# Kernel optimization log

Measured on AMD Instinct MI355X. Metric: run time of the kernel, lower is better.

The kernel has to match this reference:

```python
import jax, jax.numpy as jnp
import numpy as np

NQ = 8
NL = 6
DIM = 2 ** NQ
C64 = jnp.complex64
I2 = jnp.eye(2, dtype=C64)
PX = jnp.array([[0., 1.], [1., 0.]], dtype=C64)
PY = jnp.array([[0., -1j], [1j, 0.]], dtype=C64)
PZ = jnp.array([[1., 0.], [0., -1.]], dtype=C64)
# sign of Pauli-Z eigenvalue for each computational basis state, wires 0..3 (wire 0 = MSB)
_idx = np.arange(DIM)
_SIGNS = jnp.asarray(np.stack([1.0 - 2.0 * ((_idx >> (NQ - 1 - w)) & 1) for w in range(4)]).astype(np.float32))  # (4, 256)

def _rot(t, P):
    # exp(-i t/2 P) = cos(t/2) I - i sin(t/2) P
    th = t.astype(jnp.float32) / 2
    return jnp.cos(th) * I2 - 1j * jnp.sin(th) * P

def _apply1(st, U, w):
    # apply 2x2 unitary U on wire w; st: (B, 2,2,...,2)
    s = jnp.moveaxis(st, w + 1, -1)
    return jnp.moveaxis(s @ U.T, -1, w + 1)

def _cnot(st, c, t):
    # flip target axis where control bit == 1
    s = jnp.moveaxis(st, (c + 1, t + 1), (1, 2))
    s = jnp.concatenate([s[:, :1], s[:, 1:, ::-1]], axis=1)
    return jnp.moveaxis(s, (1, 2), (c + 1, t + 1))

def _quantum(x, weights):
    B = x.shape[0]
    # AmplitudeEmbedding with normalize=True
    psi = (x / jnp.linalg.norm(x, axis=1, keepdims=True)).astype(C64)
    st = psi.reshape((B,) + (2,) * NQ)
    for l in range(NL):
        lw = weights[l]
        for q in range(NQ):
            st = _apply1(st, _rot(lw[3 * q], PX), q)
            st = _apply1(st, _rot(lw[3 * q + 1], PY), q)
            st = _apply1(st, _rot(lw[3 * q + 2], PZ), q)
        for i in range(NQ - 1):
            st = _cnot(st, i, i + 1)
        st = _cnot(st, NQ - 1, 0)
        for i in range(0, NQ, 2):
            if i + 2 < NQ:
                st = _cnot(st, i, i + 2)
    probs = jnp.abs(st.reshape(B, DIM)) ** 2
    return probs @ _SIGNS.T  # (B, 4) Z expectations on wires 0..3

def _bn(h, g, b):
    # BatchNorm1d, training mode (batch statistics, biased variance)
    m = h.mean(0)
    v = h.var(0)
    return g * (h - m) * jax.lax.rsqrt(v + 1e-5) + b

def _forward(x, q_weights, aW, ab, fW1, fb1, fW2, fb2, cW1, cb1, g1, be1, cW2, cb2, g2, be2, cW3, cb3, cW4, cb4):
    q = _quantum(x, q_weights)                     # (B, 4)
    qf = q @ aW.T + ab                             # quantum_adapter
    cf = jnp.tanh(jax.nn.relu(x @ fW1.T + fb1) @ fW2.T + fb2)  # feature_processor
    h = qf + cf
    h = jax.nn.relu(_bn(h @ cW1.T + cb1, g1, be1))
    h = jax.nn.relu(_bn(h @ cW2.T + cb2, g2, be2))
    h = jax.nn.relu(h @ cW3.T + cb3)
    return jax.nn.sigmoid(h @ cW4.T + cb4)         # (B, 1)

def setup_inputs():
    key = jax.random.key(0)
    ks = jax.random.split(key, 21)
    f32 = jnp.float32
    r = lambda k, shp, s: jax.random.normal(k, shp, dtype=f32) * s
    B = 8192
    return {
        'x': r(ks[0], (B, 256), 1.0),
        'q_weights': r(ks[1], (NL, NQ * 3), 1.0),
        'aW': r(ks[2], (4, 4), 0.5), 'ab': r(ks[3], (4,), 0.1),
        'fW1': r(ks[4], (64, 256), 0.0625), 'fb1': r(ks[5], (64,), 0.05),
        'fW2': r(ks[6], (4, 64), 0.125), 'fb2': r(ks[7], (4,), 0.05),
        'cW1': r(ks[8], (32, 4), 0.5), 'cb1': r(ks[9], (32,), 0.05),
        'g1': 1.0 + r(ks[10], (32,), 0.05), 'be1': r(ks[11], (32,), 0.05),
        'cW2': r(ks[12], (16, 32), 0.18), 'cb2': r(ks[13], (16,), 0.05),
        'g2': 1.0 + r(ks[14], (16,), 0.05), 'be2': r(ks[15], (16,), 0.05),
        'cW3': r(ks[16], (8, 16), 0.25), 'cb3': r(ks[17], (8,), 0.05),
        'cW4': r(ks[18], (1, 8), 0.35), 'cb4': r(ks[19], (1,), 0.05),
    }

def reference(x, q_weights, aW, ab, fW1, fb1, fW2, fb2, cW1, cb1, g1, be1, cW2, cb2, g2, be2, cW3, cb3, cW4, cb4):
    return _forward(x, q_weights, aW, ab, fW1, fb1, fW2, fb2, cW1, cb1, g1, be1, cW2, cb2, g2, be2, cW3, cb3, cW4, cb4)
```

## Files before the change

kernel.cpp:

```cpp
#include <hip/hip_runtime.h>
#include <math.h>

#define INV_B (1.0f / 8192.0f)

typedef float  v2f  __attribute__((ext_vector_type(2)));
typedef _Float16 half8 __attribute__((ext_vector_type(8)));
typedef float  f32x4 __attribute__((ext_vector_type(4)));

struct QTables {
    int xm[6][8];
    int rm[6][8];
    int meas[4];
};
constexpr QTables make_tables() {
    QTables T{};
    int Mrow[8] = {}, Ncol[8] = {};
    for (int b = 0; b < 8; ++b) { Mrow[b] = 1 << b; Ncol[b] = 1 << b; }
    constexpr int bc[11] = {7,6,5,4,3,2,1,0,7,5,3};
    constexpr int bt[11] = {6,5,4,3,2,1,0,7,5,3,1};
    for (int l = 0; l < 6; ++l) {
        for (int w = 0; w < 8; ++w) { T.xm[l][w] = Ncol[7 - w]; T.rm[l][w] = Mrow[7 - w]; }
        for (int k = 0; k < 11; ++k) { Mrow[bt[k]] ^= Mrow[bc[k]]; Ncol[bc[k]] ^= Ncol[bt[k]]; }
    }
    for (int w = 0; w < 4; ++w) T.meas[w] = Mrow[7 - w];
    return T;
}
constexpr QTables TB = make_tables();

template<int ML>
static __device__ __forceinline__ float lanex(float v) {
    if constexpr (ML == 0) { return v; }
    else if constexpr (ML == 1) { return __int_as_float(__builtin_amdgcn_update_dpp(0, __float_as_int(v), 0xB1, 0xF, 0xF, true)); }
    else if constexpr (ML == 2) { return __int_as_float(__builtin_amdgcn_update_dpp(0, __float_as_int(v), 0x4E, 0xF, 0xF, true)); }
    else if constexpr (ML == 3) { return __int_as_float(__builtin_amdgcn_update_dpp(0, __float_as_int(v), 0x1B, 0xF, 0xF, true)); }
    else if constexpr (ML < 32) { return __int_as_float(__builtin_amdgcn_ds_swizzle(__float_as_int(v), 0x1F | (ML << 10))); }
    else { return __shfl_xor(v, ML, 64); }
}

static __device__ __forceinline__ float tanh_fast(float v) {
    const float c = fminf(fmaxf(v, -10.f), 10.f);
    const float e = __expf(2.f * c);
    return (e - 1.f) / (e + 1.f);
}

template<int XM, int RM>
static __device__ __forceinline__ void gate(v2f (&z)[4], const int lane,
                                            const float u00r, const float u00i,
                                            const float u01r, const float u01i) {
    constexpr int ML = XM >> 2, MR = XM & 3;
    constexpr int RL = RM >> 2, RR = RM & 3;
    const int pl = __popc(lane & RL) & 1;
    const float csi0 = pl ? -u00i : u00i;
    const float cpr0 = pl ? -u01r : u01r;
    const float csi1 = -csi0, cpr1 = -cpr0;
    v2f p[4];
    #pragma unroll
    for (int r = 0; r < 4; ++r) {
        p[r].x = lanex<ML>(z[r ^ MR].x);
        p[r].y = lanex<ML>(z[r ^ MR].y);
    }
    #pragma unroll
    for (int r = 0; r < 4; ++r) {
        const int pb = __builtin_popcount(r & RR) & 1;
        const float csi = pb ? csi1 : csi0;
        const float cpr = pb ? cpr1 : cpr0;
        const v2f zs = { -z[r].y, z[r].x };
        const v2f ps = { -p[r].y, p[r].x };
        z[r] = ((u00r * z[r] + csi * zs) + cpr * p[r]) + u01i * ps;
    }
}

#define XS 264
__global__ __launch_bounds__(256) void k_pre(
        const float* __restrict__ x, const float* __restrict__ qw,
        const float* __restrict__ fW1, const float* __restrict__ fb1,
        const float* __restrict__ fW2, const float* __restrict__ fb2,
        _Float16* __restrict__ Wt, float* __restrict__ cfws,
        float* __restrict__ accz) {
    const int t = threadIdx.x, b = blockIdx.x;

    if (b >= 128) {
        __shared__ float4 Us[48];
        if (t < 48) {
            const int l = t >> 3, q = t & 7;
            const float* a = qw + l * 24 + q * 3;
            const float h1 = 0.5f * a[0], h2 = 0.5f * a[1], h3 = 0.5f * a[2];
            const float c1 = cosf(h1), s1 = sinf(h1);
            const float c2 = cosf(h2), s2 = sinf(h2);
            const float c3 = cosf(h3), s3 = sinf(h3);
            const float m00r =  c1 * c2, m00i =  s1 * s2;
            const float m01r = -c1 * s2, m01i = -s1 * c2;
            float4 u;
            u.x = m00r * c3 + m00i * s3;  u.y = m00i * c3 - m00r * s3;
            u.z = m01r * c3 + m01i * s3;  u.w = m01i * c3 - m01r * s3;
            Us[t] = u;
        }
        __syncthreads();
        const int lane = t & 63, wv = t >> 6;
        const int k = (b - 128) * 4 + wv;
        v2f z[4];
        #pragma unroll
        for (int r = 0; r < 4; ++r) {
            z[r].x = (4 * lane + r == k) ? 1.f : 0.f;
            z[r].y = 0.f;
        }
#define GATE(L, W) { const float4 u = Us[(L) * 8 + (W)]; \
                     gate<TB.xm[L][W], TB.rm[L][W]>(z, lane, u.x, u.y, u.z, u.w); }
#define LAYER(L) GATE(L,0) GATE(L,1) GATE(L,2) GATE(L,3) GATE(L,4) GATE(L,5) GATE(L,6) GATE(L,7)
        LAYER(0) LAYER(1) LAYER(2) LAYER(3) LAYER(4) LAYER(5)
#undef LAYER
#undef GATE
        #pragma unroll
        for (int r = 0; r < 4; ++r) {
            const int i = 4 * lane + r;
            Wt[(long)i * 256 + k]         = (_Float16)z[r].x;
            Wt[(long)(256 + i) * 256 + k] = (_Float16)z[r].y;
        }
        return;
    }

    if (t < 16) accz[b * 16 + t] = 0.f;

    __shared__ _Float16 xl[64 * XS];
    __shared__ _Float16 wl[64 * XS];
    const long r0 = (long)b * 64;
    #pragma unroll
    for (int i = 0; i < 16; ++i) {
        const int idx = i * 256 + t;
        const int row = idx >> 6, c4 = idx & 63;
        const float4 xv = ((const float4*)(x + (r0 + row) * 256))[c4];
        _Float16* d = &xl[row * XS + c4 * 4];
        d[0] = (_Float16)xv.x; d[1] = (_Float16)xv.y;
        d[2] = (_Float16)xv.z; d[3] = (_Float16)xv.w;
        const float4 wv2 = ((const float4*)(fW1 + (long)row * 256))[c4];
        _Float16* e = &wl[row * XS + c4 * 4];
        e[0] = (_Float16)wv2.x; e[1] = (_Float16)wv2.y;
        e[2] = (_Float16)wv2.z; e[3] = (_Float16)wv2.w;
    }
    __syncthreads();

    const int lane = t & 63, w4 = t >> 6;
    const int g = lane >> 4, col = lane & 15;
    const int rloc = w4 * 16 + col;

    half8 bf[8];
    #pragma unroll
    for (int kb = 0; kb < 8; ++kb)
        bf[kb] = *(const half8*)&xl[rloc * XS + kb * 32 + g * 8];

    float accc[4] = {0.f, 0.f, 0.f, 0.f};
    #pragma unroll
    for (int jc = 0; jc < 4; ++jc) {
        f32x4 cv = {0.f, 0.f, 0.f, 0.f};
        #pragma unroll
        for (int kb = 0; kb < 8; ++kb) {
            const half8 af = *(const half8*)&wl[(jc * 16 + col) * XS + kb * 32 + g * 8];
            cv = __builtin_amdgcn_mfma_f32_16x16x32_f16(af, bf[kb], cv, 0, 0, 0);
        }
        #pragma unroll
        for (int r = 0; r < 4; ++r) {
            const int j = jc * 16 + g * 4 + r;
            const float z = fmaxf(cv[r] + fb1[j], 0.f);
            #pragma unroll
            for (int c = 0; c < 4; ++c) accc[c] += z * fW2[c * 64 + j];
        }
    }
    #pragma unroll
    for (int c = 0; c < 4; ++c) {
        accc[c] += __shfl_xor(accc[c], 16, 64);
        accc[c] += __shfl_xor(accc[c], 32, 64);
    }
    if (g == 0) {
        float4 o;
        o.x = tanh_fast(accc[0] + fb2[0]);
        o.y = tanh_fast(accc[1] + fb2[1]);
        o.z = tanh_fast(accc[2] + fb2[2]);
        o.w = tanh_fast(accc[3] + fb2[3]);
        ((float4*)cfws)[r0 + w4 * 16 + col] = o;
    }
}

__global__ __launch_bounds__(128) void k_gemm(
        const float* __restrict__ x, const _Float16* __restrict__ Wt,
        const float* __restrict__ cfws,
        const float* __restrict__ aW, const float* __restrict__ ab,
        float* __restrict__ hws, float* __restrict__ acc1) {
    const int t = threadIdx.x;
    const int lane = t & 63, w = t >> 6;
    const int col = lane & 15, quad = lane >> 4;
    const int R0 = blockIdx.x * 32;

    __shared__ _Float16 xa[32 * XS];
    #pragma unroll
    for (int i = 0; i < 16; ++i) {
        const int idx = i * 128 + t;
        const int row = idx >> 6, c4 = idx & 63;
        const float4 xv = ((const float4*)(x + (long)(R0 + row) * 256))[c4];
        _Float16* d = &xa[row * XS + c4 * 4];
        d[0] = (_Float16)xv.x; d[1] = (_Float16)xv.y;
        d[2] = (_Float16)xv.z; d[3] = (_Float16)xv.w;
    }
    __syncthreads();

    half8 af[8];
    #pragma unroll
    for (int kb = 0; kb < 8; ++kb)
        af[kb] = *(const half8*)&xa[(w * 16 + col) * XS + kb * 32 + quad * 8];

    int slm[4];
    #pragma unroll
    for (int mw = 0; mw < 4; ++mw) slm[mw] = __popc(col & TB.meas[mw]) & 1;

    float sS[4] = {0.f, 0.f, 0.f, 0.f};
    float sq[4][4] = {{0.f}};
    const _Float16* bre = Wt + (long)col * 256;
    const _Float16* bim = Wt + (long)(256 + col) * 256;

    #pragma unroll
    for (int c = 0; c < 16; ++c) {
        f32x4 cr0 = {0.f,0.f,0.f,0.f}, cr1 = {0.f,0.f,0.f,0.f};
        f32x4 ci0 = {0.f,0.f,0.f,0.f}, ci1 = {0.f,0.f,0.f,0.f};
        const long rowoff = (long)(c * 16) * 256 + quad * 8;
        #pragma unroll
        for (int kb = 0; kb < 4; ++kb) {
            const half8 br = *(const half8*)(bre + rowoff + kb * 32);
            cr0 = __builtin_amdgcn_mfma_f32_16x16x32_f16(af[kb], br, cr0, 0, 0, 0);
            const half8 bi = *(const half8*)(bim + rowoff + kb * 32);
            ci0 = __builtin_amdgcn_mfma_f32_16x16x32_f16(af[kb], bi, ci0, 0, 0, 0);
            const half8 br2 = *(const half8*)(bre + rowoff + (kb + 4) * 32);
            cr1 = __builtin_amdgcn_mfma_f32_16x16x32_f16(af[kb + 4], br2, cr1, 0, 0, 0);
            const half8 bi2 = *(const half8*)(bim + rowoff + (kb + 4) * 32);
            ci1 = __builtin_amdgcn_mfma_f32_16x16x32_f16(af[kb + 4], bi2, ci1, 0, 0, 0);
        }
        float sgn[4];
        #pragma unroll
        for (int mw = 0; mw < 4; ++mw) {
            const int scw = __builtin_popcount((c * 16) & TB.meas[mw]) & 1;
            sgn[mw] = (slm[mw] ^ scw) ? -1.f : 1.f;
        }
        #pragma unroll
        for (int r = 0; r < 4; ++r) {
            const float re = cr0[r] + cr1[r], im = ci0[r] + ci1[r];
            const float p = re * re + im * im;
            sS[r] += p;
            #pragma unroll
            for (int mw = 0; mw < 4; ++mw) sq[mw][r] = fmaf(sgn[mw], p, sq[mw][r]);
        }
    }

    #pragma unroll
    for (int r = 0; r < 4; ++r) {
        sS[r] += lanex<1>(sS[r]); sS[r] += lanex<2>(sS[r]);
        sS[r] += lanex<4>(sS[r]); sS[r] += lanex<8>(sS[r]);
        #pragma unroll
        for (int mw = 0; mw < 4; ++mw) {
            sq[mw][r] += lanex<1>(sq[mw][r]); sq[mw][r] += lanex<2>(sq[mw][r]);
            sq[mw][r] += lanex<4>(sq[mw][r]); sq[mw][r] += lanex<8>(sq[mw][r]);
        }
    }

    __shared__ float hb[32][4];
    if (col == 0) {
        #pragma unroll
        for (int r = 0; r < 4; ++r) {
            const int mloc = w * 16 + quad * 4 + r;
            const int row = R0 + mloc;
            const float inv = 1.0f / sS[r];
            float qe[4];
            #pragma unroll
            for (int mw = 0; mw < 4; ++mw) qe[mw] = sq[mw][r] * inv;
            const float4 cfv = ((const float4*)cfws)[row];
            const float cf[4] = {cfv.x, cfv.y, cfv.z, cfv.w};
            float h[4];
            #pragma unroll
            for (int kk = 0; kk < 4; ++kk) {
                float s = ab[kk] + cf[kk];
                #pragma unroll
                for (int j = 0; j < 4; ++j) s += aW[kk * 4 + j] * qe[j];
                h[kk] = s;
            }
            ((float4*)hws)[row] = make_float4(h[0], h[1], h[2], h[3]);
            hb[mloc][0] = h[0]; hb[mloc][1] = h[1];
            hb[mloc][2] = h[2]; hb[mloc][3] = h[3];
        }
    }
    __syncthreads();
    if (t < 20) {
        const int j = (t - 4) >> 2, kk = (t - 4) & 3;
        float v = 0.f;
        for (int rr = 0; rr < 32; ++rr)
            v += (t < 4) ? hb[rr][t] : hb[rr][j] * hb[rr][kk];
        atomicAdd(acc1 + (blockIdx.x & 31) * 20 + t, v);
    }
}

__global__ __launch_bounds__(64) void k_mid(
        const float* __restrict__ hws, const float* __restrict__ acc1,
        const float* __restrict__ cW1, const float* __restrict__ cb1,
        const float* __restrict__ g1, const float* __restrict__ be1,
        const float* __restrict__ cW2, const float* __restrict__ cb2,
        float* __restrict__ z2ws, float* __restrict__ acc2) {
    const int t = threadIdx.x;
    __shared__ float sA[20];
    __shared__ float m1s[32], is1[32];
    if (t < 20) {
        float s = 0.f;
        for (int sl = 0; sl < 32; ++sl) s += acc1[sl * 20 + t];
        sA[t] = s;
    }
    __syncthreads();
    if (t < 32) {
        float mu[4], w[4];
        #pragma unroll
        for (int k = 0; k < 4; ++k) mu[k] = sA[k] * INV_B;
        float m = cb1[t];
        #pragma unroll
        for (int k = 0; k < 4; ++k) { w[k] = cW1[t * 4 + k]; m += w[k] * mu[k]; }
        float var = 0.f;
        #pragma unroll
        for (int a2 = 0; a2 < 4; ++a2)
            #pragma unroll
            for (int b2 = 0; b2 < 4; ++b2)
                var += w[a2] * w[b2] * (sA[4 + a2 * 4 + b2] * INV_B - mu[a2] * mu[b2]);
        m1s[t] = m;
        is1[t] = 1.0f / sqrtf(var + 1e-5f);
    }
    __syncthreads();

    const long e = (long)blockIdx.x * 64 + t;
    const float4 h4 = ((const float4*)hws)[e];
    const float h[4] = {h4.x, h4.y, h4.z, h4.w};
    float a1[32];
    #pragma unroll
    for (int j = 0; j < 32; ++j) {
        float zz = cb1[j];
        #pragma unroll
        for (int k = 0; k < 4; ++k) zz += cW1[j * 4 + k] * h[k];
        a1[j] = fmaxf((zz - m1s[j]) * is1[j] * g1[j] + be1[j], 0.f);
    }
    float z2[16];
    #pragma unroll
    for (int k = 0; k < 16; ++k) {
        float s = cb2[k];
        #pragma unroll
        for (int j = 0; j < 32; ++j) s += cW2[k * 32 + j] * a1[j];
        z2[k] = s;
    }
    float4* zp = (float4*)(z2ws + e * 16);
    zp[0] = make_float4(z2[0], z2[1], z2[2], z2[3]);
    zp[1] = make_float4(z2[4], z2[5], z2[6], z2[7]);
    zp[2] = make_float4(z2[8], z2[9], z2[10], z2[11]);
    zp[3] = make_float4(z2[12], z2[13], z2[14], z2[15]);

    float sv[16], sq2[16];
    #pragma unroll
    for (int k = 0; k < 16; ++k) { sv[k] = z2[k]; sq2[k] = z2[k] * z2[k]; }
    #pragma unroll
    for (int m = 1; m < 64; m <<= 1) {
        #pragma unroll
        for (int k = 0; k < 16; ++k) {
            sv[k] += __shfl_xor(sv[k], m, 64);
            sq2[k] += __shfl_xor(sq2[k], m, 64);
        }
    }
    if (t == 0) {
        float* dst = acc2 + ((int)blockIdx.x & 31) * 32;
        #pragma unroll
        for (int k = 0; k < 16; ++k) atomicAdd(dst + k, sv[k]);
        #pragma unroll
        for (int k = 0; k < 16; ++k) atomicAdd(dst + 16 + k, sq2[k]);
    }
}

__global__ __launch_bounds__(64) void k_out(
        const float* __restrict__ z2ws, const float* __restrict__ acc2,
        const float* __restrict__ g2, const float* __restrict__ be2,
        const float* __restrict__ cW3, const float* __restrict__ cb3,
        const float* __restrict__ cW4, const float* __restrict__ cb4,
        float* __restrict__ out) {
    const int t = threadIdx.x;
    __shared__ float sB[32];
    __shared__ float m2s[16], is2[16];
    if (t < 32) {
        float s = 0.f;
        for (int sl = 0; sl < 32; ++sl) s += acc2[sl * 32 + t];
        sB[t] = s;
    }
    __syncthreads();
    if (t < 16) {
        const float m = sB[t] * INV_B;
        const float var = sB[16 + t] * INV_B - m * m;
        m2s[t] = m;
        is2[t] = 1.0f / sqrtf(var + 1e-5f);
    }
    __syncthreads();

    const long e = (long)blockIdx.x * 64 + t;
    const float4* zp = (const float4*)(z2ws + e * 16);
    const float4 v0 = zp[0], v1 = zp[1], v2 = zp[2], v3 = zp[3];
    const float z2[16] = {v0.x, v0.y, v0.z, v0.w, v1.x, v1.y, v1.z, v1.w,
                          v2.x, v2.y, v2.z, v2.w, v3.x, v3.y, v3.z, v3.w};
    float a2[16];
    #pragma unroll
    for (int k = 0; k < 16; ++k)
        a2[k] = fmaxf((z2[k] - m2s[k]) * is2[k] * g2[k] + be2[k], 0.f);
    float z3[8];
    #pragma unroll
    for (int j = 0; j < 8; ++j) {
        float s = cb3[j];
        #pragma unroll
        for (int k = 0; k < 16; ++k) s += cW3[j * 16 + k] * a2[k];
        z3[j] = fmaxf(s, 0.f);
    }
    float y = cb4[0];
    #pragma unroll
    for (int j = 0; j < 8; ++j) y += cW4[j] * z3[j];
    out[e] = 1.0f / (1.0f + expf(-y));
}

extern "C" void kernel_launch(void* const* d_in, const int* in_sizes, int n_in,
                              void* d_out, int out_size, void* d_ws, size_t ws_size,
                              hipStream_t stream) {
    (void)in_sizes; (void)n_in; (void)out_size; (void)ws_size;
    const float* x   = (const float*)d_in[0];
    const float* qw  = (const float*)d_in[1];
    const float* aW  = (const float*)d_in[2];
    const float* ab  = (const float*)d_in[3];
    const float* fW1 = (const float*)d_in[4];
    const float* fb1 = (const float*)d_in[5];
    const float* fW2 = (const float*)d_in[6];
    const float* fb2 = (const float*)d_in[7];
    const float* cW1 = (const float*)d_in[8];
    const float* cb1 = (const float*)d_in[9];
    const float* g1  = (const float*)d_in[10];
    const float* be1 = (const float*)d_in[11];
    const float* cW2 = (const float*)d_in[12];
    const float* cb2 = (const float*)d_in[13];
    const float* g2  = (const float*)d_in[14];
    const float* be2 = (const float*)d_in[15];
    const float* cW3 = (const float*)d_in[16];
    const float* cb3 = (const float*)d_in[17];
    const float* cW4 = (const float*)d_in[18];
    const float* cb4 = (const float*)d_in[19];

    float* ws   = (float*)d_ws;
    float* acc1 = ws;
    float* acc2 = ws + 1024;
    float* cfws = ws + 4096;
    float* hws  = ws + 40960;
    float* z2ws = ws + 81920;
    _Float16* Wt = (_Float16*)(ws + 215040);

    k_pre <<<192, 256, 0, stream>>>(x, qw, fW1, fb1, fW2, fb2, Wt, cfws, ws);
    k_gemm<<<256, 128, 0, stream>>>(x, Wt, cfws, aW, ab, hws, acc1);
    k_mid <<<128, 64, 0, stream>>>(hws, acc1, cW1, cb1, g1, be1, cW2, cb2, z2ws, acc2);
    k_out <<<128, 64, 0, stream>>>(z2ws, acc2, g2, be2, cW3, cb3, cW4, cb4, (float*)d_out);
}
```

Baseline: 138.5 us.

## Fuse four kernels into one persistent kernel with grid-wide atomic barriers

Merges the precompute, quantum GEMM, and both batch-norm MLP stages into a single 256-block kernel. Three software grid barriers stand in for the kernel boundaries, and per-row intermediates stay in shared memory instead of round-tripping through global workspace. Each block builds one column of the circuit unitary in wave 0 while waves 1-2 compute the feature MLP, and fW1 is read straight from global instead of staged in LDS. This removes launch gaps and global traffic but relies on all 256 blocks being co-resident, and adds a memset plus spin-wait barrier costs.

```diff
diff --git a/kernel.cpp b/kernel.cpp
--- a/kernel.cpp
+++ b/kernel.cpp
@@ -70,34 +70,82 @@
     }
 }
 
+static __device__ __forceinline__ void gbar(unsigned* ctr, unsigned target) {
+    __syncthreads();
+    if (threadIdx.x == 0) {
+        __threadfence();
+        __hip_atomic_fetch_add(ctr, 1u, __ATOMIC_ACQ_REL, __HIP_MEMORY_SCOPE_AGENT);
+        while (__hip_atomic_load(ctr, __ATOMIC_ACQUIRE, __HIP_MEMORY_SCOPE_AGENT) < target)
+            __builtin_amdgcn_s_sleep(2);
+    }
+    __syncthreads();
+    __threadfence();
+}
+
 #define XS 264
-__global__ __launch_bounds__(256) void k_pre(
+
+__global__ __launch_bounds__(256) void k_fused(
         const float* __restrict__ x, const float* __restrict__ qw,
         const float* __restrict__ fW1, const float* __restrict__ fb1,
         const float* __restrict__ fW2, const float* __restrict__ fb2,
-        _Float16* __restrict__ Wt, float* __restrict__ cfws,
-        float* __restrict__ accz) {
+        const float* __restrict__ aW, const float* __restrict__ ab,
+        const float* __restrict__ cW1, const float* __restrict__ cb1,
+        const float* __restrict__ g1, const float* __restrict__ be1,
+        const float* __restrict__ cW2, const float* __restrict__ cb2,
+        const float* __restrict__ g2, const float* __restrict__ be2,
+        const float* __restrict__ cW3, const float* __restrict__ cb3,
+        const float* __restrict__ cW4, const float* __restrict__ cb4,
+        _Float16* __restrict__ Wt, float* __restrict__ acc1,
+        float* __restrict__ acc2, unsigned* __restrict__ bar,
+        float* __restrict__ out)
+{
     const int t = threadIdx.x, b = blockIdx.x;
-
-    if (b >= 128) {
-        __shared__ float4 Us[48];
-        if (t < 48) {
-            const int l = t >> 3, q = t & 7;
-            const float* a = qw + l * 24 + q * 3;
-            const float h1 = 0.5f * a[0], h2 = 0.5f * a[1], h3 = 0.5f * a[2];
-            const float c1 = cosf(h1), s1 = sinf(h1);
-            const float c2 = cosf(h2), s2 = sinf(h2);
-            const float c3 = cosf(h3), s3 = sinf(h3);
-            const float m00r =  c1 * c2, m00i =  s1 * s2;
-            const float m01r = -c1 * s2, m01i = -s1 * c2;
-            float4 u;
-            u.x = m00r * c3 + m00i * s3;  u.y = m00i * c3 - m00r * s3;
-            u.z = m01r * c3 + m01i * s3;  u.w = m01i * c3 - m01r * s3;
-            Us[t] = u;
-        }
-        __syncthreads();
-        const int lane = t & 63, wv = t >> 6;
-        const int k = (b - 128) * 4 + wv;
+    const int lane = t & 63, w = t >> 6;
+    const int R0 = b * 32;
+    const unsigned NB = gridDim.x;
+
+    __shared__ _Float16 xa[32 * XS];
+    __shared__ float4 Us[48];
+    __shared__ float cfb[32][4];
+    __shared__ float hb[32][4];
+    __shared__ float z2b[32][16];
+    __shared__ float sA[20];
+    __shared__ float m1s[32], is1[32];
+    __shared__ float sB[32];
+    __shared__ float m2s[16], is2[16];
+
+    #pragma unroll
+    for (int i = 0; i < 8; ++i) {
+        const int idx = i * 256 + t;
+        const int row = idx >> 6, c4 = idx & 63;
+        const float4 xv = ((const float4*)(x + (long)(R0 + row) * 256))[c4];
+        _Float16* d = &xa[row * XS + c4 * 4];
+        d[0] = (_Float16)xv.x; d[1] = (_Float16)xv.y;
+        d[2] = (_Float16)xv.z; d[3] = (_Float16)xv.w;
+    }
+    if (t < 48) {
+        const int l = t >> 3, q = t & 7;
+        const float* a = qw + l * 24 + q * 3;
+        const float h1 = 0.5f * a[0], h2 = 0.5f * a[1], h3 = 0.5f * a[2];
+        const float c1 = cosf(h1), s1 = sinf(h1);
+        const float c2 = cosf(h2), s2 = sinf(h2);
+        const float c3 = cosf(h3), s3 = sinf(h3);
+        const float m00r =  c1 * c2, m00i =  s1 * s2;
+        const float m01r = -c1 * s2, m01i = -s1 * c2;
+        float4 u;
+        u.x = m00r * c3 + m00i * s3;  u.y = m00i * c3 - m00r * s3;
+        u.z = m01r * c3 + m01i * s3;  u.w = m01i * c3 - m01r * s3;
+        Us[t] = u;
+    }
+    if (b < 32 && w == 3) {
+        const int l = t - 192;
+        if (l < 20) acc1[b * 20 + l] = 0.f;
+        if (l < 32) acc2[b * 32 + l] = 0.f;
+    }
+    __syncthreads();
+
+    if (w == 0) {
+        const int k = b;
         v2f z[4];
         #pragma unroll
         for (int r = 0; r < 4; ++r) {
@@ -116,172 +164,128 @@
             Wt[(long)i * 256 + k]         = (_Float16)z[r].x;
             Wt[(long)(256 + i) * 256 + k] = (_Float16)z[r].y;
         }
-        return;
-    }
-
-    if (t < 16) accz[b * 16 + t] = 0.f;
-
-    __shared__ _Float16 xl[64 * XS];
-    __shared__ _Float16 wl[64 * XS];
-    const long r0 = (long)b * 64;
-    #pragma unroll
-    for (int i = 0; i < 16; ++i) {
-        const int idx = i * 256 + t;
-        const int row = idx >> 6, c4 = idx & 63;
-        const float4 xv = ((const float4*)(x + (r0 + row) * 256))[c4];
-        _Float16* d = &xl[row * XS + c4 * 4];
-        d[0] = (_Float16)xv.x; d[1] = (_Float16)xv.y;
-        d[2] = (_Float16)xv.z; d[3] = (_Float16)xv.w;
-        const float4 wv2 = ((const float4*)(fW1 + (long)row * 256))[c4];
-        _Float16* e = &wl[row * XS + c4 * 4];
-        e[0] = (_Float16)wv2.x; e[1] = (_Float16)wv2.y;
-        e[2] = (_Float16)wv2.z; e[3] = (_Float16)wv2.w;
-    }
-    __syncthreads();
-
-    const int lane = t & 63, w4 = t >> 6;
-    const int g = lane >> 4, col = lane & 15;
-    const int rloc = w4 * 16 + col;
-
-    half8 bf[8];
-    #pragma unroll
-    for (int kb = 0; kb < 8; ++kb)
-        bf[kb] = *(const half8*)&xl[rloc * XS + kb * 32 + g * 8];
-
-    float accc[4] = {0.f, 0.f, 0.f, 0.f};
-    #pragma unroll
-    for (int jc = 0; jc < 4; ++jc) {
-        f32x4 cv = {0.f, 0.f, 0.f, 0.f};
-        #pragma unroll
-        for (int kb = 0; kb < 8; ++kb) {
-            const half8 af = *(const half8*)&wl[(jc * 16 + col) * XS + kb * 32 + g * 8];
-            cv = __builtin_amdgcn_mfma_f32_16x16x32_f16(af, bf[kb], cv, 0, 0, 0);
-        }
+    } else if (w <= 2) {
+        const int g = lane >> 4, col = lane & 15;
+        const int mt = w - 1;
+        half8 bf[8];
+        #pragma unroll
+        for (int kb = 0; kb < 8; ++kb)
+            bf[kb] = *(const half8*)&xa[(mt * 16 + col) * XS + kb * 32 + g * 8];
+        float accc[4] = {0.f, 0.f, 0.f, 0.f};
+        #pragma unroll
+        for (int jc = 0; jc < 4; ++jc) {
+            f32x4 cv = {0.f, 0.f, 0.f, 0.f};
+            #pragma unroll
+            for (int kb = 0; kb < 8; ++kb) {
+                const float* ap = fW1 + (long)(jc * 16 + col) * 256 + kb * 32 + g * 8;
+                const float4 a0 = *(const float4*)ap;
+                const float4 a1v = *(const float4*)(ap + 4);
+                half8 af;
+                af[0] = (_Float16)a0.x;  af[1] = (_Float16)a0.y;
+                af[2] = (_Float16)a0.z;  af[3] = (_Float16)a0.w;
+                af[4] = (_Float16)a1v.x; af[5] = (_Float16)a1v.y;
+                af[6] = (_Float16)a1v.z; af[7] = (_Float16)a1v.w;
+                cv = __builtin_amdgcn_mfma_f32_16x16x32_f16(af, bf[kb], cv, 0, 0, 0);
+            }
+            #pragma unroll
+            for (int r = 0; r < 4; ++r) {
+                const int j = jc * 16 + g * 4 + r;
+                const float z = fmaxf(cv[r] + fb1[j], 0.f);
+                #pragma unroll
+                for (int c = 0; c < 4; ++c) accc[c] += z * fW2[c * 64 + j];
+            }
+        }
+        #pragma unroll
+        for (int c = 0; c < 4; ++c) {
+            accc[c] += __shfl_xor(accc[c], 16, 64);
+            accc[c] += __shfl_xor(accc[c], 32, 64);
+        }
+        if (g == 0) {
+            cfb[mt * 16 + col][0] = tanh_fast(accc[0] + fb2[0]);
+            cfb[mt * 16 + col][1] = tanh_fast(accc[1] + fb2[1]);
+            cfb[mt * 16 + col][2] = tanh_fast(accc[2] + fb2[2]);
+            cfb[mt * 16 + col][3] = tanh_fast(accc[3] + fb2[3]);
+        }
+    }
+
+    gbar(bar + 0, NB);
+
+    if (t < 128) {
+        const int col = lane & 15, quad = lane >> 4;
+        half8 af[8];
+        #pragma unroll
+        for (int kb = 0; kb < 8; ++kb)
+            af[kb] = *(const half8*)&xa[(w * 16 + col) * XS + kb * 32 + quad * 8];
+
+        int slm[4];
+        #pragma unroll
+        for (int mw = 0; mw < 4; ++mw) slm[mw] = __popc(col & TB.meas[mw]) & 1;
+
+        float sS[4] = {0.f, 0.f, 0.f, 0.f};
+        float sq[4][4] = {{0.f}};
+        const _Float16* bre = Wt + (long)col * 256;
+        const _Float16* bim = Wt + (long)(256 + col) * 256;
+
+        #pragma unroll
+        for (int c = 0; c < 16; ++c) {
+            f32x4 cr0 = {0.f,0.f,0.f,0.f}, cr1 = {0.f,0.f,0.f,0.f};
+            f32x4 ci0 = {0.f,0.f,0.f,0.f}, ci1 = {0.f,0.f,0.f,0.f};
+            const long rowoff = (long)(c * 16) * 256 + quad * 8;
+            #pragma unroll
+            for (int kb = 0; kb < 4; ++kb) {
+                const half8 br = *(const half8*)(bre + rowoff + kb * 32);
+                cr0 = __builtin_amdgcn_mfma_f32_16x16x32_f16(af[kb], br, cr0, 0, 0, 0);
+                const half8 bi = *(const half8*)(bim + rowoff + kb * 32);
+                ci0 = __builtin_amdgcn_mfma_f32_16x16x32_f16(af[kb], bi, ci0, 0, 0, 0);
+                const half8 br2 = *(const half8*)(bre + rowoff + (kb + 4) * 32);
+                cr1 = __builtin_amdgcn_mfma_f32_16x16x32_f16(af[kb + 4], br2, cr1, 0, 0, 0);
+                const half8 bi2 = *(const half8*)(bim + rowoff + (kb + 4) * 32);
+                ci1 = __builtin_amdgcn_mfma_f32_16x16x32_f16(af[kb + 4], bi2, ci1, 0, 0, 0);
+            }
+            float sgn[4];
+            #pragma unroll
+            for (int mw = 0; mw < 4; ++mw) {
+                const int scw = __builtin_popcount((c * 16) & TB.meas[mw]) & 1;
+                sgn[mw] = (slm[mw] ^ scw) ? -1.f : 1.f;
+            }
+            #pragma unroll
+            for (int r = 0; r < 4; ++r) {
+                const float re = cr0[r] + cr1[r], im = ci0[r] + ci1[r];
+                const float p = re * re + im * im;
+                sS[r] += p;
+                #pragma unroll
+                for (int mw = 0; mw < 4; ++mw) sq[mw][r] = fmaf(sgn[mw], p, sq[mw][r]);
+            }
+        }
+
         #pragma unroll
         for (int r = 0; r < 4; ++r) {
-            const int j = jc * 16 + g * 4 + r;
-            const float z = fmaxf(cv[r] + fb1[j], 0.f);
-            #pragma unroll
-            for (int c = 0; c < 4; ++c) accc[c] += z * fW2[c * 64 + j];
-        }
-    }
-    #pragma unroll
-    for (int c = 0; c < 4; ++c) {
-        accc[c] += __shfl_xor(accc[c], 16, 64);
-        accc[c] += __shfl_xor(accc[c], 32, 64);
-    }
-    if (g == 0) {
-        float4 o;
-        o.x = tanh_fast(accc[0] + fb2[0]);
-        o.y = tanh_fast(accc[1] + fb2[1]);
-        o.z = tanh_fast(accc[2] + fb2[2]);
-        o.w = tanh_fast(accc[3] + fb2[3]);
-        ((float4*)cfws)[r0 + w4 * 16 + col] = o;
-    }
-}
-
-__global__ __launch_bounds__(128) void k_gemm(
-        const float* __restrict__ x, const _Float16* __restrict__ Wt,
-        const float* __restrict__ cfws,
-        const float* __restrict__ aW, const float* __restrict__ ab,
-        float* __restrict__ hws, float* __restrict__ acc1) {
-    const int t = threadIdx.x;
-    const int lane = t & 63, w = t >> 6;
-    const int col = lane & 15, quad = lane >> 4;
-    const int R0 = blockIdx.x * 32;
-
-    __shared__ _Float16 xa[32 * XS];
-    #pragma unroll
-    for (int i = 0; i < 16; ++i) {
-        const int idx = i * 128 + t;
-        const int row = idx >> 6, c4 = idx & 63;
-        const float4 xv = ((const float4*)(x + (long)(R0 + row) * 256))[c4];
-        _Float16* d = &xa[row * XS + c4 * 4];
-        d[0] = (_Float16)xv.x; d[1] = (_Float16)xv.y;
-        d[2] = (_Float16)xv.z; d[3] = (_Float16)xv.w;
-    }
-    __syncthreads();
-
-    half8 af[8];
-    #pragma unroll
-    for (int kb = 0; kb < 8; ++kb)
-        af[kb] = *(const half8*)&xa[(w * 16 + col) * XS + kb * 32 + quad * 8];
-
-    int slm[4];
-    #pragma unroll
-    for (int mw = 0; mw < 4; ++mw) slm[mw] = __popc(col & TB.meas[mw]) & 1;
-
-    float sS[4] = {0.f, 0.f, 0.f, 0.f};
-    float sq[4][4] = {{0.f}};
-    const _Float16* bre = Wt + (long)col * 256;
-    const _Float16* bim = Wt + (long)(256 + col) * 256;
-
-    #pragma unroll
-    for (int c = 0; c < 16; ++c) {
-        f32x4 cr0 = {0.f,0.f,0.f,0.f}, cr1 = {0.f,0.f,0.f,0.f};
-        f32x4 ci0 = {0.f,0.f,0.f,0.f}, ci1 = {0.f,0.f,0.f,0.f};
-        const long rowoff = (long)(c * 16) * 256 + quad * 8;
-        #pragma unroll
-        for (int kb = 0; kb < 4; ++kb) {
-            const half8 br = *(const half8*)(bre + rowoff + kb * 32);
-            cr0 = __builtin_amdgcn_mfma_f32_16x16x32_f16(af[kb], br, cr0, 0, 0, 0);
-            const half8 bi = *(const half8*)(bim + rowoff + kb * 32);
-            ci0 = __builtin_amdgcn_mfma_f32_16x16x32_f16(af[kb], bi, ci0, 0, 0, 0);
-            const half8 br2 = *(const half8*)(bre + rowoff + (kb + 4) * 32);
-            cr1 = __builtin_amdgcn_mfma_f32_16x16x32_f16(af[kb + 4], br2, cr1, 0, 0, 0);
-            const half8 bi2 = *(const half8*)(bim + rowoff + (kb + 4) * 32);
-            ci1 = __builtin_amdgcn_mfma_f32_16x16x32_f16(af[kb + 4], bi2, ci1, 0, 0, 0);
-        }
-        float sgn[4];
-        #pragma unroll
-        for (int mw = 0; mw < 4; ++mw) {
-            const int scw = __builtin_popcount((c * 16) & TB.meas[mw]) & 1;
-            sgn[mw] = (slm[mw] ^ scw) ? -1.f : 1.f;
-        }
-        #pragma unroll
-        for (int r = 0; r < 4; ++r) {
-            const float re = cr0[r] + cr1[r], im = ci0[r] + ci1[r];
-            const float p = re * re + im * im;
-            sS[r] += p;
-            #pragma unroll
-            for (int mw = 0; mw < 4; ++mw) sq[mw][r] = fmaf(sgn[mw], p, sq[mw][r]);
-        }
-    }
-
-    #pragma unroll
-    for (int r = 0; r < 4; ++r) {
-        sS[r] += lanex<1>(sS[r]); sS[r] += lanex<2>(sS[r]);
-        sS[r] += lanex<4>(sS[r]); sS[r] += lanex<8>(sS[r]);
-        #pragma unroll
-        for (int mw = 0; mw < 4; ++mw) {
-            sq[mw][r] += lanex<1>(sq[mw][r]); sq[mw][r] += lanex<2>(sq[mw][r]);
-            sq[mw][r] += lanex<4>(sq[mw][r]); sq[mw][r] += lanex<8>(sq[mw][r]);
-        }
-    }
-
-    __shared__ float hb[32][4];
-    if (col == 0) {
-        #pragma unroll
-        for (int r = 0; r < 4; ++r) {
-            const int mloc = w * 16 + quad * 4 + r;
-            const int row = R0 + mloc;
-            const float inv = 1.0f / sS[r];
-            float qe[4];
-            #pragma unroll
-            for (int mw = 0; mw < 4; ++mw) qe[mw] = sq[mw][r] * inv;
-            const float4 cfv = ((const float4*)cfws)[row];
-            const float cf[4] = {cfv.x, cfv.y, cfv.z, cfv.w};
-            float h[4];
-            #pragma unroll
-            for (int kk = 0; kk < 4; ++kk) {
-                float s = ab[kk] + cf[kk];
+            sS[r] += lanex<1>(sS[r]); sS[r] += lanex<2>(sS[r]);
+            sS[r] += lanex<4>(sS[r]); sS[r] += lanex<8>(sS[r]);
+            #pragma unroll
+            for (int mw = 0; mw < 4; ++mw) {
+                sq[mw][r] += lanex<1>(sq[mw][r]); sq[mw][r] += lanex<2>(sq[mw][r]);
+                sq[mw][r] += lanex<4>(sq[mw][r]); sq[mw][r] += lanex<8>(sq[mw][r]);
+            }
+        }
+
+        if (col == 0) {
+            #pragma unroll
+            for (int r = 0; r < 4; ++r) {
+                const int mloc = w * 16 + quad * 4 + r;
+                const float inv = 1.0f / sS[r];
+                float qe[4];
                 #pragma unroll
-                for (int j = 0; j < 4; ++j) s += aW[kk * 4 + j] * qe[j];
-                h[kk] = s;
-            }
-            ((float4*)hws)[row] = make_float4(h[0], h[1], h[2], h[3]);
-            hb[mloc][0] = h[0]; hb[mloc][1] = h[1];
-            hb[mloc][2] = h[2]; hb[mloc][3] = h[3];
+                for (int mw = 0; mw < 4; ++mw) qe[mw] = sq[mw][r] * inv;
+                const float cf[4] = {cfb[mloc][0], cfb[mloc][1], cfb[mloc][2], cfb[mloc][3]};
+                #pragma unroll
+                for (int kk = 0; kk < 4; ++kk) {
+                    float s = ab[kk] + cf[kk];
+                    #pragma unroll
+                    for (int j = 0; j < 4; ++j) s += aW[kk * 4 + j] * qe[j];
+                    hb[mloc][kk] = s;
+                }
+            }
         }
     }
     __syncthreads();
@@ -290,19 +294,11 @@
         float v = 0.f;
         for (int rr = 0; rr < 32; ++rr)
             v += (t < 4) ? hb[rr][t] : hb[rr][j] * hb[rr][kk];
-        atomicAdd(acc1 + (blockIdx.x & 31) * 20 + t, v);
-    }
-}
-
-__global__ __launch_bounds__(64) void k_mid(
-        const float* __restrict__ hws, const float* __restrict__ acc1,
-        const float* __restrict__ cW1, const float* __restrict__ cb1,
-        const float* __restrict__ g1, const float* __restrict__ be1,
-        const float* __restrict__ cW2, const float* __restrict__ cb2,
-        float* __restrict__ z2ws, float* __restrict__ acc2) {
-    const int t = threadIdx.x;
-    __shared__ float sA[20];
-    __shared__ float m1s[32], is1[32];
+        atomicAdd(acc1 + (b & 31) * 20 + t, v);
+    }
+
+    gbar(bar + 1, NB);
+
     if (t < 20) {
         float s = 0.f;
         for (int sl = 0; sl < 32; ++sl) s += acc1[sl * 20 + t];
@@ -310,77 +306,55 @@
     }
     __syncthreads();
     if (t < 32) {
-        float mu[4], w[4];
+        float mu[4], wv[4];
         #pragma unroll
         for (int k = 0; k < 4; ++k) mu[k] = sA[k] * INV_B;
         float m = cb1[t];
         #pragma unroll
-        for (int k = 0; k < 4; ++k) { w[k] = cW1[t * 4 + k]; m += w[k] * mu[k]; }
+        for (int k = 0; k < 4; ++k) { wv[k] = cW1[t * 4 + k]; m += wv[k] * mu[k]; }
         float var = 0.f;
         #pragma unroll
         for (int a2 = 0; a2 < 4; ++a2)
             #pragma unroll
             for (int b2 = 0; b2 < 4; ++b2)
-                var += w[a2] * w[b2] * (sA[4 + a2 * 4 + b2] * INV_B - mu[a2] * mu[b2]);
+                var += wv[a2] * wv[b2] * (sA[4 + a2 * 4 + b2] * INV_B - mu[a2] * mu[b2]);
         m1s[t] = m;
         is1[t] = 1.0f / sqrtf(var + 1e-5f);
     }
     __syncthreads();
 
-    const long e = (long)blockIdx.x * 64 + t;
-    const float4 h4 = ((const float4*)hws)[e];
-    const float h[4] = {h4.x, h4.y, h4.z, h4.w};
-    float a1[32];
-    #pragma unroll
-    for (int j = 0; j < 32; ++j) {
-        float zz = cb1[j];
-        #pragma unroll
-        for (int k = 0; k < 4; ++k) zz += cW1[j * 4 + k] * h[k];
-        a1[j] = fmaxf((zz - m1s[j]) * is1[j] * g1[j] + be1[j], 0.f);
-    }
-    float z2[16];
-    #pragma unroll
-    for (int k = 0; k < 16; ++k) {
-        float s = cb2[k];
-        #pragma unroll
-        for (int j = 0; j < 32; ++j) s += cW2[k * 32 + j] * a1[j];
-        z2[k] = s;
-    }
-    float4* zp = (float4*)(z2ws + e * 16);
-    zp[0] = make_float4(z2[0], z2[1], z2[2], z2[3]);
-    zp[1] = make_float4(z2[4], z2[5], z2[6], z2[7]);
-    zp[2] = make_float4(z2[8], z2[9], z2[10], z2[11]);
-    zp[3] = make_float4(z2[12], z2[13], z2[14], z2[15]);
-
-    float sv[16], sq2[16];
-    #pragma unroll
-    for (int k = 0; k < 16; ++k) { sv[k] = z2[k]; sq2[k] = z2[k] * z2[k]; }
-    #pragma unroll
-    for (int m = 1; m < 64; m <<= 1) {
-        #pragma unroll
-        for (int k = 0; k < 16; ++k) {
-            sv[k] += __shfl_xor(sv[k], m, 64);
-            sq2[k] += __shfl_xor(sq2[k], m, 64);
-        }
-    }
-    if (t == 0) {
-        float* dst = acc2 + ((int)blockIdx.x & 31) * 32;
-        #pragma unroll
-        for (int k = 0; k < 16; ++k) atomicAdd(dst + k, sv[k]);
-        #pragma unroll
-        for (int k = 0; k < 16; ++k) atomicAdd(dst + 16 + k, sq2[k]);
-    }
-}
-
-__global__ __launch_bounds__(64) void k_out(
-        const float* __restrict__ z2ws, const float* __restrict__ acc2,
-        const float* __restrict__ g2, const float* __restrict__ be2,
-        const float* __restrict__ cW3, const float* __restrict__ cb3,
-        const float* __restrict__ cW4, const float* __restrict__ cb4,
-        float* __restrict__ out) {
-    const int t = threadIdx.x;
-    __shared__ float sB[32];
-    __shared__ float m2s[16], is2[16];
+    {
+        const int row = t & 31, grp = t >> 5;
+        const float h0 = hb[row][0], h1 = hb[row][1], h2 = hb[row][2], h3 = hb[row][3];
+        float a1[32];
+        #pragma unroll
+        for (int j = 0; j < 32; ++j) {
+            float zz = cb1[j] + cW1[j * 4 + 0] * h0 + cW1[j * 4 + 1] * h1
+                              + cW1[j * 4 + 2] * h2 + cW1[j * 4 + 3] * h3;
+            a1[j] = fmaxf((zz - m1s[j]) * is1[j] * g1[j] + be1[j], 0.f);
+        }
+        #pragma unroll
+        for (int d = 0; d < 2; ++d) {
+            const int kk = grp * 2 + d;
+            float s = cb2[kk];
+            #pragma unroll
+            for (int j = 0; j < 32; ++j) s += cW2[kk * 32 + j] * a1[j];
+            z2b[row][kk] = s;
+        }
+    }
+    __syncthreads();
+    if (t < 32) {
+        const int colz = t & 15, mode = t >> 4;
+        float s = 0.f;
+        for (int rr = 0; rr < 32; ++rr) {
+            const float v = z2b[rr][colz];
+            s += mode ? v * v : v;
+        }
+        atomicAdd(acc2 + (b & 31) * 32 + mode * 16 + colz, s);
+    }
+
+    gbar(bar + 2, NB);
+
     if (t < 32) {
         float s = 0.f;
         for (int sl = 0; sl < 32; ++sl) s += acc2[sl * 32 + t];
@@ -394,28 +368,24 @@
         is2[t] = 1.0f / sqrtf(var + 1e-5f);
     }
     __syncthreads();
-
-    const long e = (long)blockIdx.x * 64 + t;
-    const float4* zp = (const float4*)(z2ws + e * 16);
-    const float4 v0 = zp[0], v1 = zp[1], v2 = zp[2], v3 = zp[3];
-    const float z2[16] = {v0.x, v0.y, v0.z, v0.w, v1.x, v1.y, v1.z, v1.w,
-                          v2.x, v2.y, v2.z, v2.w, v3.x, v3.y, v3.z, v3.w};
-    float a2[16];
-    #pragma unroll
-    for (int k = 0; k < 16; ++k)
-        a2[k] = fmaxf((z2[k] - m2s[k]) * is2[k] * g2[k] + be2[k], 0.f);
-    float z3[8];
-    #pragma unroll
-    for (int j = 0; j < 8; ++j) {
-        float s = cb3[j];
-        #pragma unroll
-        for (int k = 0; k < 16; ++k) s += cW3[j * 16 + k] * a2[k];
-        z3[j] = fmaxf(s, 0.f);
-    }
-    float y = cb4[0];
-    #pragma unroll
-    for (int j = 0; j < 8; ++j) y += cW4[j] * z3[j];
-    out[e] = 1.0f / (1.0f + expf(-y));
+    if (t < 32) {
+        float a2[16];
+        #pragma unroll
+        for (int k = 0; k < 16; ++k)
+            a2[k] = fmaxf((z2b[t][k] - m2s[k]) * is2[k] * g2[k] + be2[k], 0.f);
+        float z3[8];
+        #pragma unroll
+        for (int j = 0; j < 8; ++j) {
+            float s = cb3[j];
+            #pragma unroll
+            for (int k = 0; k < 16; ++k) s += cW3[j * 16 + k] * a2[k];
+            z3[j] = fmaxf(s, 0.f);
+        }
+        float y = cb4[0];
+        #pragma unroll
+        for (int j = 0; j < 8; ++j) y += cW4[j] * z3[j];
+        out[R0 + t] = 1.0f / (1.0f + expf(-y));
+    }
 }
 
 extern "C" void kernel_launch(void* const* d_in, const int* in_sizes, int n_in,
@@ -443,16 +413,15 @@
     const float* cW4 = (const float*)d_in[18];
     const float* cb4 = (const float*)d_in[19];
 
-    float* ws   = (float*)d_ws;
-    float* acc1 = ws;
-    float* acc2 = ws + 1024;
-    float* cfws = ws + 4096;
-    float* hws  = ws + 40960;
-    float* z2ws = ws + 81920;
+    float* ws    = (float*)d_ws;
+    float* acc1  = ws;
+    unsigned* bar = (unsigned*)(ws + 896);
+    float* acc2  = ws + 1024;
     _Float16* Wt = (_Float16*)(ws + 215040);
-
-    k_pre <<<192, 256, 0, stream>>>(x, qw, fW1, fb1, fW2, fb2, Wt, cfws, ws);
-    k_gemm<<<256, 128, 0, stream>>>(x, Wt, cfws, aW, ab, hws, acc1);
-    k_mid <<<128, 64, 0, stream>>>(hws, acc1, cW1, cb1, g1, be1, cW2, cb2, z2ws, acc2);
-    k_out <<<128, 64, 0, stream>>>(z2ws, acc2, g2, be2, cW3, cb3, cW4, cb4, (float*)d_out);
-}
+    float* outp  = (float*)d_out;
+
+    hipMemsetAsync(bar, 0, 3 * sizeof(unsigned), stream);
+    k_fused<<<256, 256, 0, stream>>>(x, qw, fW1, fb1, fW2, fb2, aW, ab,
+                                     cW1, cb1, g1, be1, cW2, cb2, g2, be2,
+                                     cW3, cb3, cW4, cb4, Wt, acc1, acc2, bar, outp);
+}
```

After: 228.1 us. 1.65x slower.
